# Optimization experiments

Measured on AMD Instinct MI355X. Metric: run time of the kernel, lower is better.

Reference implementation:

```python
import jax, jax.numpy as jnp
import numpy as np

B, D, H, W = 8, 64, 128, 64
DX = (2.0 - -0.5) / 63.0
DY = (0.5 - -0.5) / 127.0
DZ = (0.3 - -0.5) / 63.0
INV_RE = 1.0 / 1000000.0
U_INF = 1.0
L_FIELD, L_CT = 1.0, 10.0
L_CONT, L_MOM = 1.0, 1.0
L_NOSLIP, L_INLET, L_OUTLET = 10.0, 5.0, 1.0

# central first differences
def _ddx(f, d):  # along W (last dim)
    return (f[..., 2:] - f[..., :-2]) / (2.0 * d)

def _ddy(f, d):  # along H
    return (f[..., 2:, :] - f[..., :-2, :]) / (2.0 * d)

def _ddz(f, d):  # along D
    return (f[..., 2:, :, :] - f[..., :-2, :, :]) / (2.0 * d)

# second differences
def _lap_x(f, d):
    return (f[..., 2:] - 2.0 * f[..., 1:-1] + f[..., :-2]) / (d * d)

def _lap_y(f, d):
    return (f[..., 2:, :] - 2.0 * f[..., 1:-1, :] + f[..., :-2, :]) / (d * d)

def _lap_z(f, d):
    return (f[..., 2:, :, :] - 2.0 * f[..., 1:-1, :, :] + f[..., :-2, :, :]) / (d * d)

# trims: after an x-stencil we still need to trim D,H (etc.) so every
# derivative ends up on the common interior grid (D-2, H-2, W-2)
def _tx(f):
    return f[:, :, 1:-1, 1:-1, :]

def _ty(f):
    return f[:, :, 1:-1, :, 1:-1]

def _tz(f):
    return f[:, :, :, 1:-1, 1:-1]

def _tin(f):
    return f[:, :, 1:-1, 1:-1, 1:-1]


def setup_inputs() -> dict:
    key = jax.random.key(0)
    k1, k2, k3, k4, k5 = jax.random.split(key, 5)
    return {
        "field": jax.random.normal(k1, (B, 4, D, H, W), dtype=jnp.float32),
        "ct": jax.random.normal(k2, (B, 1), dtype=jnp.float32),
        "gt_field": jax.random.normal(k3, (B, 4, D, H, W), dtype=jnp.float32),
        "gt_ct": jax.random.normal(k4, (B, 1), dtype=jnp.float32),
        "sdf": jax.random.normal(k5, (B, 1, D, H, W), dtype=jnp.float32),
    }


def _total_loss(field, ct, gt_field, gt_ct, sdf):
    # --- supervised terms ---
    loss_field = jnp.mean((field - gt_field) ** 2)
    loss_ct = jnp.mean((ct - gt_ct) ** 2)

    u = field[:, 0:1]
    v = field[:, 1:2]
    w = field[:, 2:3]
    p = field[:, 3:4]

    # --- physics: continuity ---
    du_dx = _tx(_ddx(u, DX))
    dv_dy = _ty(_ddy(v, DY))
    dw_dz = _tz(_ddz(w, DZ))
    div = du_dx + dv_dy + dw_dz
    fluid = (_tin(sdf) > 0).astype(field.dtype)
    loss_cont = jnp.mean((div * fluid) ** 2)

    # --- physics: momentum ---
    u_i, v_i, w_i = _tin(u), _tin(v), _tin(w)
    du_dy = _ty(_ddy(u, DY)); du_dz = _tz(_ddz(u, DZ))
    dv_dx = _tx(_ddx(v, DX)); dv_dz = _tz(_ddz(v, DZ))
    dw_dx = _tx(_ddx(w, DX)); dw_dy = _ty(_ddy(w, DY))
    dp_dx = _tx(_ddx(p, DX)); dp_dy = _ty(_ddy(p, DY)); dp_dz = _tz(_ddz(p, DZ))
    lap_u = _tx(_lap_x(u, DX)) + _ty(_lap_y(u, DY)) + _tz(_lap_z(u, DZ))
    lap_v = _tx(_lap_x(v, DX)) + _ty(_lap_y(v, DY)) + _tz(_lap_z(v, DZ))
    lap_w = _tx(_lap_x(w, DX)) + _ty(_lap_y(w, DY)) + _tz(_lap_z(w, DZ))
    res_x = u_i * du_dx + v_i * du_dy + w_i * du_dz + dp_dx - INV_RE * lap_u
    res_y = u_i * dv_dx + v_i * dv_dy + w_i * dv_dz + dp_dy - INV_RE * lap_v
    res_z = u_i * dw_dx + v_i * dw_dy + w_i * dw_dz + dp_dz - INV_RE * lap_w
    loss_mom = jnp.mean((res_x * fluid) ** 2 + (res_y * fluid) ** 2 + (res_z * fluid) ** 2)

    # --- boundary terms ---
    solid = (sdf <= 0).astype(field.dtype)
    loss_noslip = jnp.mean((u ** 2 + v ** 2 + w ** 2) * solid)
    loss_inlet = (
        jnp.mean((u[:, :, :, :, 0] - U_INF) ** 2)
        + jnp.mean(v[:, :, :, :, 0] ** 2)
        + jnp.mean(w[:, :, :, :, 0] ** 2)
    )
    loss_outlet = (
        jnp.mean((u[:, :, :, :, -1] - u[:, :, :, :, -2]) ** 2)
        + jnp.mean((v[:, :, :, :, -1] - v[:, :, :, :, -2]) ** 2)
        + jnp.mean((w[:, :, :, :, -1] - w[:, :, :, :, -2]) ** 2)
    )

    total = (
        L_FIELD * loss_field
        + L_CT * loss_ct
        + L_CONT * loss_cont
        + L_MOM * loss_mom
        + L_NOSLIP * loss_noslip
        + L_INLET * loss_inlet
        + L_OUTLET * loss_outlet
    )
    return total


def reference(field, ct, gt_field, gt_ct, sdf):
    return _total_loss(field, ct, gt_field, gt_ct, sdf)
```

## Files before the change

### kernel.cpp

```cpp
#include <hip/hip_runtime.h>

constexpr int Bn = 8, Dn = 64, Hn = 128, Wn = 64;
constexpr int sH = Wn;
constexpr int sD = Hn * Wn;
constexpr int sC = Dn * sD;
constexpr int sB = 4 * sC;

constexpr double DXd = 2.5 / 63.0;
constexpr double DYd = 1.0 / 127.0;
constexpr double DZd = 0.8 / 63.0;

constexpr float I2DX = (float)(0.5 / DXd);
constexpr float I2DY = (float)(0.5 / DYd);
constexpr float I2DZ = (float)(0.5 / DZd);
constexpr float IDX2 = (float)(1.0 / (DXd * DXd));
constexpr float IDY2 = (float)(1.0 / (DYd * DYd));
constexpr float IDZ2 = (float)(1.0 / (DZd * DZd));
constexpr float INV_RE = 1.0e-6f;

constexpr float CF  = (float)(1.0  / (8.0 * 4.0 * 64.0 * 128.0 * 64.0));
constexpr float CCT = (float)(10.0 / 8.0);
constexpr float CCM = (float)(1.0  / (8.0 * 62.0 * 126.0 * 62.0));
constexpr float CN  = (float)(10.0 / (8.0 * 64.0 * 128.0 * 64.0));
constexpr float CI  = (float)(5.0  / (8.0 * 64.0 * 128.0));
constexpr float CO  = (float)(1.0  / (8.0 * 64.0 * 128.0));

__device__ __forceinline__ float4 ld4(const float* __restrict__ p, int off) {
    return *reinterpret_cast<const float4*>(p + off);
}

__global__ __launch_bounds__(128, 2) void fno3d_main(
    const float* __restrict__ field,
    const float* __restrict__ gt_field,
    const float* __restrict__ sdf,
    float* __restrict__ partials)
{
    const int x   = threadIdx.x;
    const int ty  = threadIdx.y;
    const int blk = blockIdx.x;
    const int b   = blk >> 7;
    const int rem = blk & 127;
    const int d0  = (rem >> 4) << 3;
    const int h   = ((rem & 15) << 3) + ty;
    const int w0  = x << 2;

    const float* Fb = field    + b * sB;
    const float* Gb = gt_field + b * sB;
    const float* Sb = sdf      + b * sC;

    const int hm = (h > 0)      ? h - 1 : h;
    const int hp = (h < Hn - 1) ? h + 1 : h;
    const bool hIn = (h >= 1) & (h <= Hn - 2);

    const int rowc = h  * sH + w0;
    const int rowm = hm * sH + w0;
    const int rowp = hp * sH + w0;

    const int dm0 = (d0 > 0) ? d0 - 1 : 0;
    const int dn0 = (d0 < Dn - 1) ? d0 + 1 : d0;

    float4 pU = ld4(Fb, dm0 * sD + rowc);
    float4 pV = ld4(Fb, sC + dm0 * sD + rowc);
    float4 pW = ld4(Fb, 2 * sC + dm0 * sD + rowc);
    float4 pP = ld4(Fb, 3 * sC + dm0 * sD + rowc);
    float4 cU = ld4(Fb, d0 * sD + rowc);
    float4 cV = ld4(Fb, sC + d0 * sD + rowc);
    float4 cW = ld4(Fb, 2 * sC + d0 * sD + rowc);
    float4 cP = ld4(Fb, 3 * sC + d0 * sD + rowc);
    float4 nU = ld4(Fb, dn0 * sD + rowc);
    float4 nV = ld4(Fb, sC + dn0 * sD + rowc);
    float4 nW = ld4(Fb, 2 * sC + dn0 * sD + rowc);
    float4 nP = ld4(Fb, 3 * sC + dn0 * sD + rowc);

    float4 yUm = ld4(Fb, d0 * sD + rowm), yUp = ld4(Fb, d0 * sD + rowp);
    float4 yVm = ld4(Fb, sC + d0 * sD + rowm), yVp = ld4(Fb, sC + d0 * sD + rowp);
    float4 yWm = ld4(Fb, 2 * sC + d0 * sD + rowm), yWp = ld4(Fb, 2 * sC + d0 * sD + rowp);
    float4 yPm = ld4(Fb, 3 * sC + d0 * sD + rowm), yPp = ld4(Fb, 3 * sC + d0 * sD + rowp);

    float4 gU = ld4(Gb, d0 * sD + rowc);
    float4 gV = ld4(Gb, sC + d0 * sD + rowc);
    float4 gW = ld4(Gb, 2 * sC + d0 * sD + rowc);
    float4 gP = ld4(Gb, 3 * sC + d0 * sD + rowc);
    float4 sS = ld4(Sb, d0 * sD + rowc);

    float acc = 0.f;

    #pragma unroll
    for (int k = 0; k < 8; ++k) {
        const int d   = d0 + k;
        const int dn  = (d  < Dn - 1) ? d  + 1 : d;
        const int dnn = (dn < Dn - 1) ? dn + 1 : dn;

        const float4 qU = ld4(Fb, dnn * sD + rowc);
        const float4 qV = ld4(Fb, sC + dnn * sD + rowc);
        const float4 qW = ld4(Fb, 2 * sC + dnn * sD + rowc);
        const float4 qP = ld4(Fb, 3 * sC + dnn * sD + rowc);

        const float4 zUm = ld4(Fb, dn * sD + rowm), zUp = ld4(Fb, dn * sD + rowp);
        const float4 zVm = ld4(Fb, sC + dn * sD + rowm), zVp = ld4(Fb, sC + dn * sD + rowp);
        const float4 zWm = ld4(Fb, 2 * sC + dn * sD + rowm), zWp = ld4(Fb, 2 * sC + dn * sD + rowp);
        const float4 zPm = ld4(Fb, 3 * sC + dn * sD + rowm), zPp = ld4(Fb, 3 * sC + dn * sD + rowp);

        const float4 hGU = ld4(Gb, dn * sD + rowc);
        const float4 hGV = ld4(Gb, sC + dn * sD + rowc);
        const float4 hGW = ld4(Gb, 2 * sC + dn * sD + rowc);
        const float4 hGP = ld4(Gb, 3 * sC + dn * sD + rowc);
        const float4 hS  = ld4(Sb, dn * sD + rowc);

        const float uLs = __shfl_up(cU.w, 1), uRs = __shfl_down(cU.x, 1);
        const float vLs = __shfl_up(cV.w, 1), vRs = __shfl_down(cV.x, 1);
        const float wLs = __shfl_up(cW.w, 1), wRs = __shfl_down(cW.x, 1);
        const float pLs = __shfl_up(cP.w, 1), pRs = __shfl_down(cP.x, 1);

        const float* au = (const float*)&cU; const float* av = (const float*)&cV;
        const float* aw = (const float*)&cW; const float* ap = (const float*)&cP;
        const float* apu = (const float*)&pU; const float* apv = (const float*)&pV;
        const float* apw = (const float*)&pW; const float* app = (const float*)&pP;
        const float* anu = (const float*)&nU; const float* anv = (const float*)&nV;
        const float* anw = (const float*)&nW; const float* anp = (const float*)&nP;
        const float* agu = (const float*)&gU; const float* agv = (const float*)&gV;
        const float* agw = (const float*)&gW; const float* agp = (const float*)&gP;
        const float* as_ = (const float*)&sS;
        const float* ayum = (const float*)&yUm; const float* ayup = (const float*)&yUp;
        const float* ayvm = (const float*)&yVm; const float* ayvp = (const float*)&yVp;
        const float* aywm = (const float*)&yWm; const float* aywp = (const float*)&yWp;
        const float* aypm = (const float*)&yPm; const float* aypp = (const float*)&yPp;

        const bool dIn = (d >= 1) & (d <= Dn - 2);

        #pragma unroll
        for (int e = 0; e < 4; ++e) {
            const int w = w0 + e;
            const float u = au[e], v = av[e], wq = aw[e], pq = ap[e];

            {
                const float e0 = u  - agu[e];
                const float e1 = v  - agv[e];
                const float e2 = wq - agw[e];
                const float e3 = pq - agp[e];
                acc += CF * (e0 * e0 + e1 * e1 + e2 * e2 + e3 * e3);
            }

            const float s = as_[e];

            acc += ((s <= 0.f) ? CN : 0.f) * (u * u + v * v + wq * wq);

            {
                const float du = u - 1.0f;
                acc += ((w == 0) ? CI : 0.f) * (du * du + v * v + wq * wq);
            }

            const float uxm = (e == 0) ? uLs : au[e - 1];
            const float uxp = (e == 3) ? uRs : au[e + 1];
            const float vxm = (e == 0) ? vLs : av[e - 1];
            const float vxp = (e == 3) ? vRs : av[e + 1];
            const float wxm = (e == 0) ? wLs : aw[e - 1];
            const float wxp = (e == 3) ? wRs : aw[e + 1];
            const float pxm = (e == 0) ? pLs : ap[e - 1];
            const float pxp = (e == 3) ? pRs : ap[e + 1];

            const float du_dx = (uxp - uxm) * I2DX;
            const float du_dy = (ayup[e] - ayum[e]) * I2DY;
            const float du_dz = (anu[e] - apu[e]) * I2DZ;
            const float dv_dx = (vxp - vxm) * I2DX;
            const float dv_dy = (ayvp[e] - ayvm[e]) * I2DY;
            const float dv_dz = (anv[e] - apv[e]) * I2DZ;
            const float dw_dx = (wxp - wxm) * I2DX;
            const float dw_dy = (aywp[e] - aywm[e]) * I2DY;
            const float dw_dz = (anw[e] - apw[e]) * I2DZ;
            const float dp_dx = (pxp - pxm) * I2DX;
            const float dp_dy = (aypp[e] - aypm[e]) * I2DY;
            const float dp_dz = (anp[e] - app[e]) * I2DZ;

            const float div = du_dx + dv_dy + dw_dz;

            const float lap_u = (uxp - 2.f * u  + uxm) * IDX2 + (ayup[e] - 2.f * u  + ayum[e]) * IDY2 + (anu[e] - 2.f * u  + apu[e]) * IDZ2;
            const float lap_v = (vxp - 2.f * v  + vxm) * IDX2 + (ayvp[e] - 2.f * v  + ayvm[e]) * IDY2 + (anv[e] - 2.f * v  + apv[e]) * IDZ2;
            const float lap_w = (wxp - 2.f * wq + wxm) * IDX2 + (aywp[e] - 2.f * wq + aywm[e]) * IDY2 + (anw[e] - 2.f * wq + apw[e]) * IDZ2;

            const float rx = u * du_dx + v * du_dy + wq * du_dz + dp_dx - INV_RE * lap_u;
            const float ry = u * dv_dx + v * dv_dy + wq * dv_dz + dp_dy - INV_RE * lap_v;
            const float rz = u * dw_dx + v * dw_dy + wq * dw_dz + dp_dz - INV_RE * lap_w;

            const bool wIn = (w >= 1) & (w <= Wn - 2);
            const float m = (s > 0.f && wIn && hIn && dIn) ? CCM : 0.f;
            acc += m * (div * div + rx * rx + ry * ry + rz * rz);
        }

        if (x == 15) {
            const float a0 = au[3] - au[2];
            const float a1 = av[3] - av[2];
            const float a2 = aw[3] - aw[2];
            acc += CO * (a0 * a0 + a1 * a1 + a2 * a2);
        }

        pU = cU; pV = cV; pW = cW; pP = cP;
        cU = nU; cV = nV; cW = nW; cP = nP;
        nU = qU; nV = qV; nW = qW; nP = qP;
        yUm = zUm; yUp = zUp; yVm = zVm; yVp = zVp;
        yWm = zWm; yWp = zWp; yPm = zPm; yPp = zPp;
        gU = hGU; gV = hGV; gW = hGW; gP = hGP;
        sS = hS;
    }

    for (int off = 32; off > 0; off >>= 1)
        acc += __shfl_down(acc, off);

    __shared__ float wsum[2];
    const int tid  = threadIdx.y * 16 + threadIdx.x;
    const int wid  = tid >> 6;
    const int lane = tid & 63;
    if (lane == 0) wsum[wid] = acc;
    __syncthreads();
    if (tid == 0) partials[blk] = wsum[0] + wsum[1];
}

__global__ __launch_bounds__(256) void fno3d_reduce(
    const float* __restrict__ partials,
    const float* __restrict__ ct,
    const float* __restrict__ gt_ct,
    float* __restrict__ out)
{
    const int t = threadIdx.x;
    float s = partials[t] + partials[t + 256] + partials[t + 512] + partials[t + 768];
    for (int off = 32; off > 0; off >>= 1)
        s += __shfl_down(s, off);

    __shared__ float wsum[4];
    if ((t & 63) == 0) wsum[t >> 6] = s;
    __syncthreads();
    if (t == 0) {
        float tot = wsum[0] + wsum[1] + wsum[2] + wsum[3];
        float ctl = 0.f;
        for (int i = 0; i < Bn; ++i) {
            const float dc = ct[i] - gt_ct[i];
            ctl += dc * dc;
        }
        out[0] = tot + CCT * ctl;
    }
}

extern "C" void kernel_launch(void* const* d_in, const int* in_sizes, int n_in,
                              void* d_out, int out_size, void* d_ws, size_t ws_size,
                              hipStream_t stream) {
    const float* field    = (const float*)d_in[0];
    const float* ct       = (const float*)d_in[1];
    const float* gt_field = (const float*)d_in[2];
    const float* gt_ct    = (const float*)d_in[3];
    const float* sdf      = (const float*)d_in[4];
    float* out      = (float*)d_out;
    float* partials = (float*)d_ws;

    hipLaunchKernelGGL(fno3d_main, dim3(1024), dim3(16, 8, 1), 0, stream,
                       field, gt_field, sdf, partials);
    hipLaunchKernelGGL(fno3d_reduce, dim3(1), dim3(256), 0, stream,
                       partials, ct, gt_ct, out);
}
```

Before: 172.4 us.

## Stage field planes into LDS via async global_load_lds with ring buffer

Replaces per-thread register loads of the center, z-neighbor and y-halo rows with a 4-slot LDS ring buffer. Core rows are filled by direct global-to-LDS DMA and the y-halo rows by ordinary loads written to LDS. Stencil neighbors are then read from LDS, so each plane is fetched from global memory once per block instead of several times. The cost is manual vmcnt waits and two barriers per depth step. The hard-coded wait counts could be fragile if the compiler reorders or merges loads.

```diff
diff --git a/kernel.cpp b/kernel.cpp
--- a/kernel.cpp
+++ b/kernel.cpp
@@ -1,15 +1,14 @@
 #include <hip/hip_runtime.h>
 
 constexpr int Bn = 8, Dn = 64, Hn = 128, Wn = 64;
-constexpr int sH = Wn;
-constexpr int sD = Hn * Wn;
-constexpr int sC = Dn * sD;
-constexpr int sB = 4 * sC;
+constexpr int sH = 64;
+constexpr int sD = 8192;
+constexpr int sC = 524288;
+constexpr int sB = 2097152;
 
 constexpr double DXd = 2.5 / 63.0;
 constexpr double DYd = 1.0 / 127.0;
 constexpr double DZd = 0.8 / 63.0;
-
 constexpr float I2DX = (float)(0.5 / DXd);
 constexpr float I2DY = (float)(0.5 / DYd);
 constexpr float I2DZ = (float)(0.5 / DZd);
@@ -25,108 +24,155 @@
 constexpr float CI  = (float)(5.0  / (8.0 * 64.0 * 128.0));
 constexpr float CO  = (float)(1.0  / (8.0 * 64.0 * 128.0));
 
-__device__ __forceinline__ float4 ld4(const float* __restrict__ p, int off) {
+__device__ __forceinline__ float4 ld4(const float* p, int off) {
     return *reinterpret_cast<const float4*>(p + off);
 }
 
-__global__ __launch_bounds__(128, 2) void fno3d_main(
+__device__ __forceinline__ void dma16(const float* g, float* l) {
+    __builtin_amdgcn_global_load_lds(
+        (const __attribute__((address_space(1))) void*)g,
+        (__attribute__((address_space(3))) void*)l,
+        16, 0, 0);
+}
+
+__global__ __launch_bounds__(128) void fno3d_main(
     const float* __restrict__ field,
     const float* __restrict__ gt_field,
     const float* __restrict__ sdf,
     float* __restrict__ partials)
 {
-    const int x   = threadIdx.x;
-    const int ty  = threadIdx.y;
+    __shared__ float lds[4][4][10][64];
+
+    const int tid = threadIdx.x;
+    const int x   = tid & 15;
+    const int ty  = (tid >> 4) & 7;
+    const int wv  = tid >> 6;
+    const int lx  = tid & 63;
+
     const int blk = blockIdx.x;
     const int b   = blk >> 7;
     const int rem = blk & 127;
     const int d0  = (rem >> 4) << 3;
-    const int h   = ((rem & 15) << 3) + ty;
+    const int h0  = (rem & 15) << 3;
+    const int h   = h0 + ty;
     const int w0  = x << 2;
 
     const float* Fb = field    + b * sB;
     const float* Gb = gt_field + b * sB;
     const float* Sb = sdf      + b * sC;
 
-    const int hm = (h > 0)      ? h - 1 : h;
-    const int hp = (h < Hn - 1) ? h + 1 : h;
-    const bool hIn = (h >= 1) & (h <= Hn - 2);
-
-    const int rowc = h  * sH + w0;
-    const int rowm = hm * sH + w0;
-    const int rowp = hp * sH + w0;
-
-    const int dm0 = (d0 > 0) ? d0 - 1 : 0;
-    const int dn0 = (d0 < Dn - 1) ? d0 + 1 : d0;
-
-    float4 pU = ld4(Fb, dm0 * sD + rowc);
-    float4 pV = ld4(Fb, sC + dm0 * sD + rowc);
-    float4 pW = ld4(Fb, 2 * sC + dm0 * sD + rowc);
-    float4 pP = ld4(Fb, 3 * sC + dm0 * sD + rowc);
-    float4 cU = ld4(Fb, d0 * sD + rowc);
-    float4 cV = ld4(Fb, sC + d0 * sD + rowc);
-    float4 cW = ld4(Fb, 2 * sC + d0 * sD + rowc);
-    float4 cP = ld4(Fb, 3 * sC + d0 * sD + rowc);
-    float4 nU = ld4(Fb, dn0 * sD + rowc);
-    float4 nV = ld4(Fb, sC + dn0 * sD + rowc);
-    float4 nW = ld4(Fb, 2 * sC + dn0 * sD + rowc);
-    float4 nP = ld4(Fb, 3 * sC + dn0 * sD + rowc);
-
-    float4 yUm = ld4(Fb, d0 * sD + rowm), yUp = ld4(Fb, d0 * sD + rowp);
-    float4 yVm = ld4(Fb, sC + d0 * sD + rowm), yVp = ld4(Fb, sC + d0 * sD + rowp);
-    float4 yWm = ld4(Fb, 2 * sC + d0 * sD + rowm), yWp = ld4(Fb, 2 * sC + d0 * sD + rowp);
-    float4 yPm = ld4(Fb, 3 * sC + d0 * sD + rowm), yPp = ld4(Fb, 3 * sC + d0 * sD + rowp);
-
-    float4 gU = ld4(Gb, d0 * sD + rowc);
-    float4 gV = ld4(Gb, sC + d0 * sD + rowc);
-    float4 gW = ld4(Gb, 2 * sC + d0 * sD + rowc);
-    float4 gP = ld4(Gb, 3 * sC + d0 * sD + rowc);
-    float4 sS = ld4(Sb, d0 * sD + rowc);
+    const int hmg = (h0 > 0) ? h0 - 1 : 0;
+    const int hpg = (h0 + 8 < Hn) ? h0 + 8 : Hn - 1;
+    const int rowc = h * sH + w0;
+    const bool hIn = (h >= 1) && (h <= Hn - 2);
+
+    const int hch    = (tid >> 4) & 3;
+    const int hwhich = tid >> 6;
+    const int hrow   = hwhich ? hpg : hmg;
+
+    auto stage_core = [&](int p, int s) {
+        #pragma unroll
+        for (int c = 0; c < 4; ++c) {
+            const int ch   = (wv << 1) | (c >> 1);
+            const int half = c & 1;
+            const float* g = Fb + ch * sC + p * sD
+                           + (h0 + half * 4 + (lx >> 4)) * sH + ((lx & 15) << 2);
+            dma16(g, &lds[s][ch][1 + half * 4][0]);
+        }
+    };
+    auto load_halo = [&](int p) {
+        return ld4(Fb, hch * sC + p * sD + hrow * sH + w0);
+    };
+
+    stage_core((d0 > 0) ? d0 - 1 : 0, 3);
+    stage_core(d0, 0);
+    stage_core(d0 + 1, 1);
+
+    float4 gtb[2][4], sdb[2], hb[2];
+    gtb[0][0] = ld4(Gb, d0 * sD + rowc);
+    gtb[0][1] = ld4(Gb, sC + d0 * sD + rowc);
+    gtb[0][2] = ld4(Gb, 2 * sC + d0 * sD + rowc);
+    gtb[0][3] = ld4(Gb, 3 * sC + d0 * sD + rowc);
+    sdb[0]    = ld4(Sb, d0 * sD + rowc);
+    hb[0] = load_halo(d0);
+    hb[1] = load_halo(d0 + 1);
+    *(float4*)&lds[0][hch][hwhich * 9][w0] = hb[0];
 
     float acc = 0.f;
 
     #pragma unroll
     for (int k = 0; k < 8; ++k) {
-        const int d   = d0 + k;
-        const int dn  = (d  < Dn - 1) ? d  + 1 : d;
-        const int dnn = (dn < Dn - 1) ? dn + 1 : dn;
-
-        const float4 qU = ld4(Fb, dnn * sD + rowc);
-        const float4 qV = ld4(Fb, sC + dnn * sD + rowc);
-        const float4 qW = ld4(Fb, 2 * sC + dnn * sD + rowc);
-        const float4 qP = ld4(Fb, 3 * sC + dnn * sD + rowc);
-
-        const float4 zUm = ld4(Fb, dn * sD + rowm), zUp = ld4(Fb, dn * sD + rowp);
-        const float4 zVm = ld4(Fb, sC + dn * sD + rowm), zVp = ld4(Fb, sC + dn * sD + rowp);
-        const float4 zWm = ld4(Fb, 2 * sC + dn * sD + rowm), zWp = ld4(Fb, 2 * sC + dn * sD + rowp);
-        const float4 zPm = ld4(Fb, 3 * sC + dn * sD + rowm), zPp = ld4(Fb, 3 * sC + dn * sD + rowp);
-
-        const float4 hGU = ld4(Gb, dn * sD + rowc);
-        const float4 hGV = ld4(Gb, sC + dn * sD + rowc);
-        const float4 hGW = ld4(Gb, 2 * sC + dn * sD + rowc);
-        const float4 hGP = ld4(Gb, 3 * sC + dn * sD + rowc);
-        const float4 hS  = ld4(Sb, dn * sD + rowc);
+        const int d  = d0 + k;
+        const int sc = k & 3, sp = (k + 3) & 3, sn = (k + 1) & 3;
+
+        if (k < 7) {
+            const int d1 = (d + 1 < Dn) ? d + 1 : Dn - 1;
+            gtb[(k + 1) & 1][0] = ld4(Gb, d1 * sD + rowc);
+            gtb[(k + 1) & 1][1] = ld4(Gb, sC + d1 * sD + rowc);
+            gtb[(k + 1) & 1][2] = ld4(Gb, 2 * sC + d1 * sD + rowc);
+            gtb[(k + 1) & 1][3] = ld4(Gb, 3 * sC + d1 * sD + rowc);
+            sdb[(k + 1) & 1]    = ld4(Sb, d1 * sD + rowc);
+        }
+        if (k < 6) {
+            const int d2 = (d + 2 < Dn) ? d + 2 : Dn - 1;
+            hb[k & 1] = load_halo(d2);
+        }
+        if (k < 7) {
+            const int d2 = (d + 2 < Dn) ? d + 2 : Dn - 1;
+            stage_core(d2, (k + 2) & 3);
+        }
+        if (k <= 6) {
+            *(float4*)&lds[sn][hch][hwhich * 9][w0] = hb[(k + 1) & 1];
+        }
+
+        if (k < 6)       asm volatile("s_waitcnt vmcnt(10) lgkmcnt(0)" ::: "memory");
+        else if (k == 6) asm volatile("s_waitcnt vmcnt(9) lgkmcnt(0)" ::: "memory");
+        else             asm volatile("s_waitcnt vmcnt(0) lgkmcnt(0)" ::: "memory");
+        __builtin_amdgcn_s_barrier();
+
+        const float4 cU  = *(const float4*)&lds[sc][0][1 + ty][w0];
+        const float4 cV  = *(const float4*)&lds[sc][1][1 + ty][w0];
+        const float4 cW  = *(const float4*)&lds[sc][2][1 + ty][w0];
+        const float4 cP  = *(const float4*)&lds[sc][3][1 + ty][w0];
+        const float4 zpU = *(const float4*)&lds[sp][0][1 + ty][w0];
+        const float4 zpV = *(const float4*)&lds[sp][1][1 + ty][w0];
+        const float4 zpW = *(const float4*)&lds[sp][2][1 + ty][w0];
+        const float4 zpP = *(const float4*)&lds[sp][3][1 + ty][w0];
+        const float4 znU = *(const float4*)&lds[sn][0][1 + ty][w0];
+        const float4 znV = *(const float4*)&lds[sn][1][1 + ty][w0];
+        const float4 znW = *(const float4*)&lds[sn][2][1 + ty][w0];
+        const float4 znP = *(const float4*)&lds[sn][3][1 + ty][w0];
+        const float4 yUm = *(const float4*)&lds[sc][0][ty][w0];
+        const float4 yUp = *(const float4*)&lds[sc][0][2 + ty][w0];
+        const float4 yVm = *(const float4*)&lds[sc][1][ty][w0];
+        const float4 yVp = *(const float4*)&lds[sc][1][2 + ty][w0];
+        const float4 yWm = *(const float4*)&lds[sc][2][ty][w0];
+        const float4 yWp = *(const float4*)&lds[sc][2][2 + ty][w0];
+        const float4 yPm = *(const float4*)&lds[sc][3][ty][w0];
+        const float4 yPp = *(const float4*)&lds[sc][3][2 + ty][w0];
 
         const float uLs = __shfl_up(cU.w, 1), uRs = __shfl_down(cU.x, 1);
         const float vLs = __shfl_up(cV.w, 1), vRs = __shfl_down(cV.x, 1);
         const float wLs = __shfl_up(cW.w, 1), wRs = __shfl_down(cW.x, 1);
         const float pLs = __shfl_up(cP.w, 1), pRs = __shfl_down(cP.x, 1);
 
-        const float* au = (const float*)&cU; const float* av = (const float*)&cV;
-        const float* aw = (const float*)&cW; const float* ap = (const float*)&cP;
-        const float* apu = (const float*)&pU; const float* apv = (const float*)&pV;
-        const float* apw = (const float*)&pW; const float* app = (const float*)&pP;
-        const float* anu = (const float*)&nU; const float* anv = (const float*)&nV;
-        const float* anw = (const float*)&nW; const float* anp = (const float*)&nP;
-        const float* agu = (const float*)&gU; const float* agv = (const float*)&gV;
-        const float* agw = (const float*)&gW; const float* agp = (const float*)&gP;
-        const float* as_ = (const float*)&sS;
+        const float* au = (const float*)&cU;  const float* av = (const float*)&cV;
+        const float* aw = (const float*)&cW;  const float* ap = (const float*)&cP;
+        const float* apu = (const float*)&zpU; const float* apv = (const float*)&zpV;
+        const float* apw = (const float*)&zpW; const float* app = (const float*)&zpP;
+        const float* anu = (const float*)&znU; const float* anv = (const float*)&znV;
+        const float* anw = (const float*)&znW; const float* anp = (const float*)&znP;
         const float* ayum = (const float*)&yUm; const float* ayup = (const float*)&yUp;
         const float* ayvm = (const float*)&yVm; const float* ayvp = (const float*)&yVp;
         const float* aywm = (const float*)&yWm; const float* aywp = (const float*)&yWp;
         const float* aypm = (const float*)&yPm; const float* aypp = (const float*)&yPp;
-
-        const bool dIn = (d >= 1) & (d <= Dn - 2);
+        const float* agu = (const float*)&gtb[k & 1][0];
+        const float* agv = (const float*)&gtb[k & 1][1];
+        const float* agw = (const float*)&gtb[k & 1][2];
+        const float* agp = (const float*)&gtb[k & 1][3];
+        const float* as_ = (const float*)&sdb[k & 1];
+
+        const bool dIn = (d >= 1) && (d <= Dn - 2);
 
         #pragma unroll
         for (int e = 0; e < 4; ++e) {
@@ -142,7 +188,6 @@
             }
 
             const float s = as_[e];
-
             acc += ((s <= 0.f) ? CN : 0.f) * (u * u + v * v + wq * wq);
 
             {
@@ -182,7 +227,7 @@
             const float ry = u * dv_dx + v * dv_dy + wq * dv_dz + dp_dy - INV_RE * lap_v;
             const float rz = u * dw_dx + v * dw_dy + wq * dw_dz + dp_dz - INV_RE * lap_w;
 
-            const bool wIn = (w >= 1) & (w <= Wn - 2);
+            const bool wIn = (w >= 1) && (w <= Wn - 2);
             const float m = (s > 0.f && wIn && hIn && dIn) ? CCM : 0.f;
             acc += m * (div * div + rx * rx + ry * ry + rz * rz);
         }
@@ -194,25 +239,15 @@
             acc += CO * (a0 * a0 + a1 * a1 + a2 * a2);
         }
 
-        pU = cU; pV = cV; pW = cW; pP = cP;
-        cU = nU; cV = nV; cW = nW; cP = nP;
-        nU = qU; nV = qV; nW = qW; nP = qP;
-        yUm = zUm; yUp = zUp; yVm = zVm; yVp = zVp;
-        yWm = zWm; yWp = zWp; yPm = zPm; yPp = zPp;
-        gU = hGU; gV = hGV; gW = hGW; gP = hGP;
-        sS = hS;
+        __builtin_amdgcn_s_barrier();
     }
 
     for (int off = 32; off > 0; off >>= 1)
         acc += __shfl_down(acc, off);
-
-    __shared__ float wsum[2];
-    const int tid  = threadIdx.y * 16 + threadIdx.x;
-    const int wid  = tid >> 6;
-    const int lane = tid & 63;
-    if (lane == 0) wsum[wid] = acc;
     __syncthreads();
-    if (tid == 0) partials[blk] = wsum[0] + wsum[1];
+    if ((tid & 63) == 0) ((float*)lds)[wv] = acc;
+    __syncthreads();
+    if (tid == 0) partials[blk] = ((float*)lds)[0] + ((float*)lds)[1];
 }
 
 __global__ __launch_bounds__(256) void fno3d_reduce(
@@ -251,7 +286,7 @@
     float* out      = (float*)d_out;
     float* partials = (float*)d_ws;
 
-    hipLaunchKernelGGL(fno3d_main, dim3(1024), dim3(16, 8, 1), 0, stream,
+    hipLaunchKernelGGL(fno3d_main, dim3(1024), dim3(128), 0, stream,
                        field, gt_field, sdf, partials);
     hipLaunchKernelGGL(fno3d_reduce, dim3(1), dim3(256), 0, stream,
                        partials, ct, gt_ct, out);
```

Result: no change. 174.0 us (+0.9%).
